# Kernel tuning notes

Hardware: AMD Instinct MI355X
Metric: run time of the kernel (lower is better)

## Reference

```python
import jax, jax.numpy as jnp
import numpy as np

TEMP = 0.07
POS_WINDOW = 2
EPS = 1e-8
NEG = -1e9  # finite large-negative for masking (safe under vjp)


def _l2norm(x):
    # matches F.normalize(dim=-1) with eps=1e-12
    n = jnp.sqrt(jnp.sum(x * x, axis=-1, keepdims=True))
    return x / jnp.maximum(n, 1e-12)


def setup_inputs() -> dict:
    key = jax.random.key(0)
    k1, k2, k3, k4, k5 = jax.random.split(key, 5)
    B, T, D = 32, 1024, 256
    eeg_enc = jax.random.normal(k1, (B, T, D), dtype=jnp.float32)
    eye_enc = jax.random.normal(k2, (B, T, D), dtype=jnp.float32)
    mask = jax.random.randint(k3, (B, T), 0, 2, dtype=jnp.int32)
    W_eeg = jax.random.normal(k4, (D, D), dtype=jnp.float32) / np.sqrt(D)
    W_eye = jax.random.normal(k5, (D, D), dtype=jnp.float32) / np.sqrt(D)
    return {"eeg_enc": eeg_enc, "eye_enc": eye_enc, "mask": mask,
            "W_eeg": W_eeg, "W_eye": W_eye}


def reference(eeg_enc, eye_enc, mask, W_eeg, W_eye):
    B, T, D = eeg_enc.shape
    valid = mask > 0  # (B,T)
    # nn.Linear(bias=False): x @ W.T, then L2-normalize
    e = _l2norm(jnp.einsum('btd,ed->bte', eeg_enc, W_eeg))
    v = _l2norm(jnp.einsum('btd,ed->bte', eye_enc, W_eye))
    sims = jnp.einsum('bid,bjd->bij', e, v) / TEMP  # (B,T,T)
    # rank of each valid step within the compressed (gathered) ordering
    rank = jnp.cumsum(valid.astype(jnp.int32), axis=-1) - 1  # (B,T)
    band = jnp.abs(rank[:, :, None] - rank[:, None, :]) <= POS_WINDOW
    pair = valid[:, :, None] & valid[:, None, :]  # both steps valid
    pos = pair & band
    # per-row max over positive (banded) entries
    pos_scores = jnp.max(jnp.where(pos, sims, NEG), axis=-1)  # (B,T)
    # logsumexp over valid columns (the gathered sims row)
    lse = jax.nn.logsumexp(jnp.where(valid[:, None, :], sims, NEG), axis=-1)
    row_loss = -(pos_scores - lse)  # (B,T)
    Tv = jnp.sum(valid, axis=-1)  # (B,)
    per_b = jnp.sum(jnp.where(valid, row_loss, 0.0), axis=-1) / jnp.maximum(Tv, 1)
    per_b = jnp.where(Tv >= 2, per_b, 0.0)  # skip samples with <2 valid steps
    return jnp.sum(per_b) / (B + EPS)
```

## Files before the change

### kernel.cpp

```cpp
#include <hip/hip_runtime.h>
#include <hip/hip_bf16.h>

typedef __attribute__((ext_vector_type(8))) short bf16x8;
typedef __attribute__((ext_vector_type(4))) float f32x4;

#define INVT (1.0f/0.07f)

static __device__ __forceinline__ short f2bf(float f){
    unsigned int u = __float_as_uint(f);
    unsigned int r = (u + 0x7fffu + ((u >> 16) & 1u)) >> 16;
    return (short)r;
}
static __device__ __forceinline__ float bf2f(short s){
    return __uint_as_float(((unsigned int)(unsigned short)s) << 16);
}

static __device__ __forceinline__ void gld16(const void* g, void* l){
    __builtin_amdgcn_global_load_lds(
        (const __attribute__((address_space(1))) unsigned int*)g,
        (__attribute__((address_space(3))) unsigned int*)l, 16, 0, 0);
}

__global__ __launch_bounds__(256) void prep_kernel(const float* __restrict__ Weeg,
                                                   const float* __restrict__ Weye,
                                                   const int* __restrict__ mask,
                                                   short* __restrict__ Wout,
                                                   int* __restrict__ rank,
                                                   int* __restrict__ idx,
                                                   int* __restrict__ Tv,
                                                   float* __restrict__ cb,
                                                   float* __restrict__ bsum){
    __shared__ int ssum[256];
    int tid = threadIdx.x;
    if (blockIdx.x < 512){
        int i = blockIdx.x * 256 + tid;
        float v = (i < 65536) ? Weeg[i] : Weye[i - 65536];
        Wout[i] = f2bf(v);
        return;
    }
    int b = blockIdx.x - 512;
    if (tid == 0) bsum[b] = 0.f;
    int local[4]; int s = 0;
    #pragma unroll
    for (int q = 0; q < 4; ++q){
        int t = tid*4 + q;
        local[q] = (mask[b*1024 + t] > 0) ? 1 : 0;
        s += local[q];
    }
    ssum[tid] = s;
    __syncthreads();
    for (int off = 1; off < 256; off <<= 1){
        int add = (tid >= off) ? ssum[tid - off] : 0;
        __syncthreads();
        ssum[tid] += add;
        __syncthreads();
    }
    int run = ssum[tid] - s;
    #pragma unroll
    for (int q = 0; q < 4; ++q){
        int t = tid*4 + q;
        int g = b*1024 + t;
        run += local[q];
        rank[g] = run - 1;
        cb[g]   = local[q] ? 0.0f : -1e9f;
        if (local[q]) idx[b*1024 + run - 1] = t;
    }
    if (tid == 255) Tv[b] = ssum[255];
}

__global__ __launch_bounds__(256, 5) void proj_kernel(const float* __restrict__ Aeeg,
                                                      const float* __restrict__ Aeye,
                                                      const short* __restrict__ Wbf,
                                                      short* __restrict__ Eout,
                                                      short* __restrict__ Vout){
    __shared__ short sW[64 * 256];
    int sel = blockIdx.y;
    const float* A   = sel ? Aeye : Aeeg;
    const short* W   = Wbf + sel * 65536;
    short*       Out = sel ? Vout : Eout;

    int tid = threadIdx.x;
    int w = tid >> 6, lane = tid & 63;
    int l15 = lane & 15, lq = lane >> 4;
    int kb  = lq * 8;
    int row0 = blockIdx.x * 64;

    bf16x8 xf[8];
    {
        const float* ap = A + (size_t)(row0 + w*16 + l15) * 256 + kb;
        #pragma unroll
        for (int g = 0; g < 8; ++g){
            float4 x0 = *(const float4*)(ap + g*32);
            float4 x1 = *(const float4*)(ap + g*32 + 4);
            bf16x8 t;
            t[0]=f2bf(x0.x); t[1]=f2bf(x0.y); t[2]=f2bf(x0.z); t[3]=f2bf(x0.w);
            t[4]=f2bf(x1.x); t[5]=f2bf(x1.y); t[6]=f2bf(x1.z); t[7]=f2bf(x1.w);
            xf[g] = t;
        }
    }

    f32x4 acc[16];
    #pragma unroll
    for (int q = 0; q < 16; ++q) acc[q] = (f32x4){0.f,0.f,0.f,0.f};

    int ro   = lane >> 5;
    int cb_s = lane & 31;
    int s7   = l15 & 7;

    #pragma unroll
    for (int pass = 0; pass < 4; ++pass){
        if (pass) __syncthreads();
        #pragma unroll
        for (int p = 0; p < 8; ++p){
            int rl  = w*16 + p*2 + ro;
            int cbg = cb_s ^ ((p*2 + ro) & 7);
            gld16(W + (size_t)(pass*64 + rl)*256 + cbg*8,
                  &sW[(w*16 + p*2) * 256]);
        }
        __syncthreads();
        #pragma unroll
        for (int nt = 0; nt < 4; ++nt){
            f32x4 c = acc[pass*4 + nt];
            int rbase = (nt*16 + l15) * 256;
            #pragma unroll
            for (int g = 0; g < 8; ++g){
                bf16x8 wf = *(const bf16x8*)&sW[rbase + (((g*4 + lq) ^ s7) << 3)];
                c = __builtin_amdgcn_mfma_f32_16x16x32_bf16(wf, xf[g], c, 0, 0, 0);
            }
            acc[pass*4 + nt] = c;
        }
    }

    float ss = 0.f;
    #pragma unroll
    for (int q = 0; q < 16; ++q){
        #pragma unroll
        for (int r = 0; r < 4; ++r){ float x = acc[q][r]; ss += x*x; }
    }
    ss += __shfl_xor(ss, 16);
    ss += __shfl_xor(ss, 32);
    float scale = 1.0f / fmaxf(sqrtf(ss), 1e-12f);

    short* op = Out + (size_t)(row0 + w*16 + l15) * 256 + lq*4;
    #pragma unroll
    for (int q = 0; q < 16; ++q){
        short4 pk;
        pk.x = f2bf(acc[q][0] * scale);
        pk.y = f2bf(acc[q][1] * scale);
        pk.z = f2bf(acc[q][2] * scale);
        pk.w = f2bf(acc[q][3] * scale);
        *(short4*)(op + ((q >> 2) * 64 + (q & 3) * 16)) = pk;
    }
}

__global__ __launch_bounds__(256, 5) void loss_kernel(const short* __restrict__ E,
                                                      const short* __restrict__ V,
                                                      const float* __restrict__ cb,
                                                      float* __restrict__ psum){
    __shared__ short sE[128 * 64];
    __shared__ short sV[128 * 64];

    int n  = blockIdx.x;
    int m  = n >> 3;
    int b  = ((m >> 6) << 3) | (n & 7);
    int lm = m & 63;
    int i0 = (lm >> 3) * 128;
    int jb = lm & 7;
    int j0 = jb * 128;

    int tid = threadIdx.x;
    int w = tid >> 6, lane = tid & 63;
    int wi = w >> 1, wj = w & 1;
    int l15 = lane & 15, lq = lane >> 4;
    int s7 = l15 & 7;

    int swz = ((lane & 7) ^ (lane >> 3)) * 8;
    const short* Eg = E + ((size_t)b*1024 + i0 + w*32 + (lane>>3))*256 + swz;
    const short* Vg = V + ((size_t)b*1024 + j0 + w*32 + (lane>>3))*256 + swz;
    short* sEw = &sE[(w*32)*64];
    short* sVw = &sV[(w*32)*64];

    float cbv[4];
    #pragma unroll
    for (int jj = 0; jj < 4; ++jj)
        cbv[jj] = cb[b*1024 + j0 + wj*64 + jj*16 + l15];

    f32x4 acc[4][4];
    #pragma unroll
    for (int ii = 0; ii < 4; ++ii)
        #pragma unroll
        for (int jj = 0; jj < 4; ++jj) acc[ii][jj] = (f32x4){0.f,0.f,0.f,0.f};

    #pragma unroll
    for (int kc = 0; kc < 4; ++kc){
        __syncthreads();
        #pragma unroll
        for (int p = 0; p < 4; ++p){
            gld16(Eg + kc*64 + p*2048, sEw + p*512);
            gld16(Vg + kc*64 + p*2048, sVw + p*512);
        }
        __syncthreads();

        #pragma unroll
        for (int ks = 0; ks < 2; ++ks){
            bf16x8 af[4], bf[4];
            #pragma unroll
            for (int t = 0; t < 4; ++t){
                int co = (((ks*4 + lq) ^ s7)) << 3;
                af[t] = *(const bf16x8*)&sE[(wi*64 + t*16 + l15)*64 + co];
                bf[t] = *(const bf16x8*)&sV[(wj*64 + t*16 + l15)*64 + co];
            }
            #pragma unroll
            for (int ii = 0; ii < 4; ++ii)
                #pragma unroll
                for (int jj = 0; jj < 4; ++jj)
                    acc[ii][jj] = __builtin_amdgcn_mfma_f32_16x16x32_bf16(af[ii], bf[jj], acc[ii][jj], 0, 0, 0);
        }
    }

    float ls[4][4];
    #pragma unroll
    for (int ii = 0; ii < 4; ++ii){
        #pragma unroll
        for (int r = 0; r < 4; ++r){
            float s = 0.f;
            #pragma unroll
            for (int jj = 0; jj < 4; ++jj)
                s += __expf(fmaf(acc[ii][jj][r], INVT, cbv[jj]));
            ls[ii][r] = s;
        }
    }
    #pragma unroll
    for (int ii = 0; ii < 4; ++ii){
        #pragma unroll
        for (int r = 0; r < 4; ++r){
            float v = ls[ii][r];
            v += __shfl_xor(v, 1);
            v += __shfl_xor(v, 2);
            v += __shfl_xor(v, 4);
            v += __shfl_xor(v, 8);
            ls[ii][r] = v;
        }
    }
    float myv = ls[0][0];
    #pragma unroll
    for (int q = 1; q < 16; ++q)
        if (l15 == q) myv = ls[q>>2][q&3];
    int slice = jb*2 + wj;
    float* pp = psum + (((size_t)(b*16 + slice)) << 10);
    pp[i0 + wi*64 + lq*4 + (l15>>2)*16 + (l15&3)] = myv;
}

__global__ __launch_bounds__(256) void pos_kernel(const short* __restrict__ E,
                                                  const short* __restrict__ V,
                                                  const int* __restrict__ mask,
                                                  const int* __restrict__ rank,
                                                  const int* __restrict__ idx,
                                                  const int* __restrict__ Tv,
                                                  float* __restrict__ pmax){
    int tid = threadIdx.x;
    int gl  = tid & 15;
    int rf  = (blockIdx.x * 256 + tid) >> 4;
    int b   = rf >> 10;
    if (mask[rf] <= 0) return;

    int ri = rank[rf];
    int tv = Tv[b];
    int lo = ri - 2; if (lo < 0) lo = 0;
    int hi = ri + 2; if (hi > tv - 1) hi = tv - 1;

    const short* epp = E + (size_t)rf * 256 + gl * 16;
    float ev[16];
    {
        bf16x8 e0 = *(const bf16x8*)epp;
        bf16x8 e1 = *(const bf16x8*)(epp + 8);
        #pragma unroll
        for (int k = 0; k < 8; ++k){ ev[k] = bf2f(e0[k]); ev[8+k] = bf2f(e1[k]); }
    }
    float pm = -1e30f;
    for (int r = lo; r <= hi; ++r){
        int j = idx[b*1024 + r];
        const short* vpp = V + ((size_t)(b*1024) + j) * 256 + gl * 16;
        bf16x8 v0 = *(const bf16x8*)vpp;
        bf16x8 v1 = *(const bf16x8*)(vpp + 8);
        float s = 0.f;
        #pragma unroll
        for (int k = 0; k < 8; ++k){
            s = fmaf(ev[k],   bf2f(v0[k]), s);
            s = fmaf(ev[8+k], bf2f(v1[k]), s);
        }
        s += __shfl_xor(s, 1);
        s += __shfl_xor(s, 2);
        s += __shfl_xor(s, 4);
        s += __shfl_xor(s, 8);
        pm = fmaxf(pm, s);
    }
    if (gl == 0) pmax[rf] = pm * INVT;
}

__global__ __launch_bounds__(256) void reduce_kernel(const float* __restrict__ psum,
                                                     const float* __restrict__ pmax,
                                                     const int* __restrict__ mask,
                                                     float* __restrict__ bsum){
    int b  = blockIdx.x >> 2;
    int i  = (blockIdx.x & 3) * 256 + threadIdx.x;
    int g  = b*1024 + i;
    float a = 0.f;
    if (mask[g] > 0){
        const float* pp = psum + ((size_t)b << 14);
        float ps = 0.f;
        #pragma unroll
        for (int s = 0; s < 16; ++s) ps += pp[i + (s << 10)];
        a = logf(ps) - pmax[g];
    }
    #pragma unroll
    for (int m = 1; m < 64; m <<= 1) a += __shfl_xor(a, m);
    if ((threadIdx.x & 63) == 0 && a != 0.f) atomicAdd(&bsum[b], a);
}

__global__ void final_kernel(const float* __restrict__ bsum,
                             const int* __restrict__ Tv,
                             float* __restrict__ out){
    int tid = threadIdx.x;
    float v = 0.f;
    if (tid < 32){
        int tv = Tv[tid];
        if (tv >= 2) v = bsum[tid] / (float)tv;
    }
    #pragma unroll
    for (int m = 1; m < 64; m <<= 1) v += __shfl_xor(v, m);
    if (tid == 0) out[0] = v / 32.0f;
}

extern "C" void kernel_launch(void* const* d_in, const int* in_sizes, int n_in,
                              void* d_out, int out_size, void* d_ws, size_t ws_size,
                              hipStream_t stream) {
    const float* eeg  = (const float*)d_in[0];
    const float* eye  = (const float*)d_in[1];
    const int*   mask = (const int*)d_in[2];
    const float* Weeg = (const float*)d_in[3];
    const float* Weye = (const float*)d_in[4];
    float* out = (float*)d_out;

    char* ws = (char*)d_ws;
    short* e_bf  = (short*)(ws);
    short* v_bf  = (short*)(ws + 16777216);
    short* wbf   = (short*)(ws + 33554432);
    int*   rank  = (int*)  (ws + 33816576);
    int*   idx   = (int*)  (ws + 33947648);
    float* cb    = (float*)(ws + 34078720);
    float* psum  = (float*)(ws + 34209792);
    float* pmax  = (float*)(ws + 36306944);
    int*   Tv    = (int*)  (ws + 36438016);
    float* bsum  = (float*)(ws + 36438144);

    prep_kernel<<<544, 256, 0, stream>>>(Weeg, Weye, mask, wbf, rank, idx, Tv, cb, bsum);
    proj_kernel<<<dim3(512, 2), 256, 0, stream>>>(eeg, eye, wbf, e_bf, v_bf);
    loss_kernel<<<2048, 256, 0, stream>>>(e_bf, v_bf, cb, psum);
    pos_kernel<<<2048, 256, 0, stream>>>(e_bf, v_bf, mask, rank, idx, Tv, pmax);
    reduce_kernel<<<128, 256, 0, stream>>>(psum, pmax, mask, bsum);
    final_kernel<<<1, 64, 0, stream>>>(bsum, Tv, out);
}
```

Before: 173.2 us.

## Restructure loss kernel: register-resident E rows, full-K V tiles double-buffered in LDS

```diff
diff --git a/kernel.cpp b/kernel.cpp
--- a/kernel.cpp
+++ b/kernel.cpp
@@ -153,12 +153,12 @@
     }
 }
 
-__global__ __launch_bounds__(256, 5) void loss_kernel(const short* __restrict__ E,
+__global__ __launch_bounds__(256, 2) void loss_kernel(const short* __restrict__ E,
                                                       const short* __restrict__ V,
                                                       const float* __restrict__ cb,
                                                       float* __restrict__ psum){
-    __shared__ short sE[128 * 64];
-    __shared__ short sV[128 * 64];
+    __shared__ short sV[2][64 * 256];
+    __shared__ float sRed[4][32];
 
     int n  = blockIdx.x;
     int m  = n >> 3;
@@ -170,85 +170,102 @@
 
     int tid = threadIdx.x;
     int w = tid >> 6, lane = tid & 63;
-    int wi = w >> 1, wj = w & 1;
     int l15 = lane & 15, lq = lane >> 4;
+    int kb = lq * 8;
     int s7 = l15 & 7;
 
-    int swz = ((lane & 7) ^ (lane >> 3)) * 8;
-    const short* Eg = E + ((size_t)b*1024 + i0 + w*32 + (lane>>3))*256 + swz;
-    const short* Vg = V + ((size_t)b*1024 + j0 + w*32 + (lane>>3))*256 + swz;
-    short* sEw = &sE[(w*32)*64];
-    short* sVw = &sV[(w*32)*64];
-
-    float cbv[4];
-    #pragma unroll
-    for (int jj = 0; jj < 4; ++jj)
-        cbv[jj] = cb[b*1024 + j0 + wj*64 + jj*16 + l15];
-
-    f32x4 acc[4][4];
-    #pragma unroll
-    for (int ii = 0; ii < 4; ++ii)
-        #pragma unroll
-        for (int jj = 0; jj < 4; ++jj) acc[ii][jj] = (f32x4){0.f,0.f,0.f,0.f};
-
-    #pragma unroll
-    for (int kc = 0; kc < 4; ++kc){
-        __syncthreads();
-        #pragma unroll
-        for (int p = 0; p < 4; ++p){
-            gld16(Eg + kc*64 + p*2048, sEw + p*512);
-            gld16(Vg + kc*64 + p*2048, sVw + p*512);
-        }
-        __syncthreads();
-
-        #pragma unroll
-        for (int ks = 0; ks < 2; ++ks){
-            bf16x8 af[4], bf[4];
+    int ro = lane >> 5;
+    int cs = lane & 31;
+    const short* Vrow = V + ((size_t)b*1024 + j0 + w*16 + ro) * 256;
+    #pragma unroll
+    for (int p = 0; p < 8; ++p){
+        int rr = (p*2 + ro) & 7;
+        gld16(Vrow + (size_t)(p*2)*256 + (size_t)((cs ^ rr) * 8),
+              &sV[0][(w*16 + p*2) * 256]);
+    }
+
+    bf16x8 af[2][8];
+    {
+        const short* ep = E + ((size_t)b*1024 + i0 + w*32 + l15) * 256 + kb;
+        #pragma unroll
+        for (int g = 0; g < 8; ++g){
+            af[0][g] = *(const bf16x8*)(ep + g*32);
+            af[1][g] = *(const bf16x8*)(ep + 16*256 + g*32);
+        }
+    }
+
+    float cbv[8];
+    #pragma unroll
+    for (int ct = 0; ct < 8; ++ct)
+        cbv[ct] = cb[b*1024 + j0 + ct*16 + l15];
+
+    f32x4 acc[2][8];
+    #pragma unroll
+    for (int s = 0; s < 2; ++s)
+        #pragma unroll
+        for (int ct = 0; ct < 8; ++ct) acc[s][ct] = (f32x4){0.f,0.f,0.f,0.f};
+
+    __syncthreads();
+
+    #pragma unroll
+    for (int p = 0; p < 8; ++p){
+        int rr = (p*2 + ro) & 7;
+        gld16(Vrow + (size_t)(64 + p*2)*256 + (size_t)((cs ^ rr) * 8),
+              &sV[1][(w*16 + p*2) * 256]);
+    }
+
+    #pragma unroll
+    for (int jt = 0; jt < 4; ++jt){
+        bf16x8 bf[8];
+        #pragma unroll
+        for (int g = 0; g < 8; ++g)
+            bf[g] = *(const bf16x8*)&sV[0][(jt*16 + l15)*256 + (((g*4 + lq) ^ s7) << 3)];
+        #pragma unroll
+        for (int g = 0; g < 8; ++g){
+            acc[0][jt] = __builtin_amdgcn_mfma_f32_16x16x32_bf16(af[0][g], bf[g], acc[0][jt], 0, 0, 0);
+            acc[1][jt] = __builtin_amdgcn_mfma_f32_16x16x32_bf16(af[1][g], bf[g], acc[1][jt], 0, 0, 0);
+        }
+    }
+
+    __syncthreads();
+
+    #pragma unroll
+    for (int jt = 0; jt < 4; ++jt){
+        bf16x8 bf[8];
+        #pragma unroll
+        for (int g = 0; g < 8; ++g)
+            bf[g] = *(const bf16x8*)&sV[1][(jt*16 + l15)*256 + (((g*4 + lq) ^ s7) << 3)];
+        #pragma unroll
+        for (int g = 0; g < 8; ++g){
+            acc[0][4+jt] = __builtin_amdgcn_mfma_f32_16x16x32_bf16(af[0][g], bf[g], acc[0][4+jt], 0, 0, 0);
+            acc[1][4+jt] = __builtin_amdgcn_mfma_f32_16x16x32_bf16(af[1][g], bf[g], acc[1][4+jt], 0, 0, 0);
+        }
+    }
+
+    float ls[2][4];
+    #pragma unroll
+    for (int s = 0; s < 2; ++s){
+        #pragma unroll
+        for (int r = 0; r < 4; ++r){
+            float acv = 0.f;
             #pragma unroll
-            for (int t = 0; t < 4; ++t){
-                int co = (((ks*4 + lq) ^ s7)) << 3;
-                af[t] = *(const bf16x8*)&sE[(wi*64 + t*16 + l15)*64 + co];
-                bf[t] = *(const bf16x8*)&sV[(wj*64 + t*16 + l15)*64 + co];
-            }
+            for (int ct = 0; ct < 8; ++ct)
+                acv += __expf(fmaf(acc[s][ct][r], INVT, cbv[ct]));
             #pragma unroll
-            for (int ii = 0; ii < 4; ++ii)
-                #pragma unroll
-                for (int jj = 0; jj < 4; ++jj)
-                    acc[ii][jj] = __builtin_amdgcn_mfma_f32_16x16x32_bf16(af[ii], bf[jj], acc[ii][jj], 0, 0, 0);
-        }
-    }
-
-    float ls[4][4];
-    #pragma unroll
-    for (int ii = 0; ii < 4; ++ii){
-        #pragma unroll
-        for (int r = 0; r < 4; ++r){
-            float s = 0.f;
+            for (int mm = 1; mm < 16; mm <<= 1)
+                acv += __shfl_xor(acv, mm);
+            ls[s][r] = acv;
+        }
+    }
+    if (l15 == 0){
+        #pragma unroll
+        for (int s = 0; s < 2; ++s)
             #pragma unroll
-            for (int jj = 0; jj < 4; ++jj)
-                s += __expf(fmaf(acc[ii][jj][r], INVT, cbv[jj]));
-            ls[ii][r] = s;
-        }
-    }
-    #pragma unroll
-    for (int ii = 0; ii < 4; ++ii){
-        #pragma unroll
-        for (int r = 0; r < 4; ++r){
-            float v = ls[ii][r];
-            v += __shfl_xor(v, 1);
-            v += __shfl_xor(v, 2);
-            v += __shfl_xor(v, 4);
-            v += __shfl_xor(v, 8);
-            ls[ii][r] = v;
-        }
-    }
-    float myv = ls[0][0];
-    #pragma unroll
-    for (int q = 1; q < 16; ++q)
-        if (l15 == q) myv = ls[q>>2][q&3];
-    int slice = jb*2 + wj;
-    float* pp = psum + (((size_t)(b*16 + slice)) << 10);
-    pp[i0 + wi*64 + lq*4 + (l15>>2)*16 + (l15&3)] = myv;
+            for (int r = 0; r < 4; ++r)
+                sRed[w][s*16 + lq*4 + r] = ls[s][r];
+    }
+    float* pp = psum + (((size_t)(b*8 + jb)) << 10);
+    if (lane < 32) pp[i0 + w*32 + lane] = sRed[w][lane];
 }
 
 __global__ __launch_bounds__(256) void pos_kernel(const short* __restrict__ E,
@@ -307,10 +324,10 @@
     int g  = b*1024 + i;
     float a = 0.f;
     if (mask[g] > 0){
-        const float* pp = psum + ((size_t)b << 14);
+        const float* pp = psum + ((size_t)b << 13);
         float ps = 0.f;
         #pragma unroll
-        for (int s = 0; s < 16; ++s) ps += pp[i + (s << 10)];
+        for (int s = 0; s < 8; ++s) ps += pp[i + (s << 10)];
         a = logf(ps) - pmax[g];
     }
     #pragma unroll
@@ -350,9 +367,9 @@
     int*   idx   = (int*)  (ws + 33947648);
     float* cb    = (float*)(ws + 34078720);
     float* psum  = (float*)(ws + 34209792);
-    float* pmax  = (float*)(ws + 36306944);
-    int*   Tv    = (int*)  (ws + 36438016);
-    float* bsum  = (float*)(ws + 36438144);
+    float* pmax  = (float*)(ws + 35258368);
+    int*   Tv    = (int*)  (ws + 35389440);
+    float* bsum  = (float*)(ws + 35389568);
 
     prep_kernel<<<544, 256, 0, stream>>>(Weeg, Weye, mask, wbf, rank, idx, Tv, cb, bsum);
     proj_kernel<<<dim3(512, 2), 256, 0, stream>>>(eeg, eye, wbf, e_bf, v_bf);
```

Measured after the change: 171.0 us. About the same (-1.3%).
